# Kernel tuning notes

Measured on AMD Instinct MI355X. Metric: run time of the kernel, lower is better.

The kernel has to match this reference:

```python
import jax, jax.numpy as jnp
import numpy as np

B, L, D, MELS, VOCAB, MAXDUR = 16, 256, 512, 80, 256, 12
T_MAX = L * MAXDUR  # 3072, upper bound on expanded mel length


def setup_inputs() -> dict:
    key = jax.random.key(0)
    ks = jax.random.split(key, 10)
    s = 1.0 / np.sqrt(D)
    return {
        "src": jax.random.randint(ks[0], (B, L), 0, VOCAB),
        "input_dur_inframe": jax.random.randint(ks[1], (B, L), 0, MAXDUR),
        "T": T_MAX,
        "emb_table": jax.random.normal(ks[2], (VOCAB, D), jnp.float32),
        "pos_table": jax.random.normal(ks[3], (L, D), jnp.float32),
        "W_enc": jax.random.normal(ks[4], (D, D), jnp.float32) * s,
        "b_enc": jnp.zeros((D,), jnp.float32),
        "W_dur": jax.random.normal(ks[5], (D, 1), jnp.float32) * s,
        "b_dur": jnp.zeros((1,), jnp.float32),
        "W_dec": jax.random.normal(ks[6], (D, D), jnp.float32) * s,
        "b_dec": jnp.zeros((D,), jnp.float32),
        "W_gen": jax.random.normal(ks[7], (D, MELS), jnp.float32) * s,
        "b_gen": jnp.zeros((MELS,), jnp.float32),
    }


def length_regulate(enc, dur, T):
    """Vectorized equivalent of the nested per-(batch, token) scatter loop.
    Frame f of batch j copies enc[j, k] where k is the token whose duration
    span covers f; frames past the total duration stay zero."""
    csum = jnp.cumsum(dur, axis=-1)                      # [B, L]
    frames = jnp.arange(T)                               # [T]
    # token index per frame: count of tokens with csum <= f
    tok = jax.vmap(lambda c: jnp.searchsorted(c, frames, side="right"))(csum)  # [B, T]
    valid = (tok < dur.shape[1])[..., None]               # [B, T, 1]
    tok = jnp.minimum(tok, dur.shape[1] - 1)
    out = jnp.take_along_axis(enc, tok[..., None], axis=1)  # [B, T, D]
    return out * valid


def reference(src, input_dur_inframe, T, emb_table, pos_table,
              W_enc, b_enc, W_dur, b_dur, W_dec, b_dec, W_gen, b_gen):
    # encode: embedding + positional embedding -> encoder
    x = emb_table[src] + pos_table[None, : src.shape[1], :]        # [B, L, D]
    enc = jax.nn.relu(x @ W_enc + b_enc)                            # [B, L, D]
    # duration predictor on encoder output
    dur_pred = (enc @ W_dur + b_dur)[..., 0]                        # [B, L]
    # length regulator (the custom-kernel hot spot)
    outp = length_regulate(enc, input_dur_inframe, T)               # [B, T, D]
    # decoder + generator, then permute to [B, n_mels, T]
    dec = jax.nn.relu(outp @ W_dec + b_dec)                         # [B, T, D]
    mel = jnp.transpose(dec @ W_gen + b_gen, (0, 2, 1))             # [B, MELS, T]
    return mel, dur_pred
```

## Files before the change

kernel.cpp:

```cpp
#include <hip/hip_runtime.h>

#define D_ 512
#define L_ 256
#define B_ 16
#define T_ 3072
#define MELS_ 80
#define R_ 4096
#define CS_ 4104

typedef __bf16 bf16x8 __attribute__((ext_vector_type(8)));
typedef float f32x4 __attribute__((ext_vector_type(4)));

__device__ __forceinline__ unsigned f2bf(float f) {
  union { float f; unsigned u; } x; x.f = f;
  return (x.u + 0x7FFFu + ((x.u >> 16) & 1u)) >> 16;
}
__device__ __forceinline__ float bf2f(unsigned h) {
  union { unsigned u; float f; } x; x.u = h << 16;
  return x.f;
}

__device__ __forceinline__ void transw_dev(const float* __restrict__ src,
                                           unsigned short* __restrict__ dst,
                                           int N, int local, float* sh) {
  int kt = local & 7, nt = local >> 3;
  int k0 = kt * 64, n0 = nt * 64;
  int tid = threadIdx.x;
  int c = tid & 63, r4 = tid >> 6;
  for (int it = 0; it < 16; ++it) {
    int r = it * 4 + r4;
    int n = n0 + c;
    sh[r * 65 + c] = (n < N) ? src[(k0 + r) * N + n] : 0.f;
  }
  __syncthreads();
  for (int it = 0; it < 16; ++it) {
    int r = it * 4 + r4;
    int n = n0 + r;
    if (n < N) dst[n * D_ + k0 + c] = (unsigned short)f2bf(sh[c * 65 + r]);
  }
}

__device__ __forceinline__ void tok_dev(const int* __restrict__ dur,
                                        int* __restrict__ TOK, int b, int* cs) {
  int tid = threadIdx.x;
  cs[tid] = dur[b * L_ + tid];
  for (int off = 1; off < L_; off <<= 1) {
    __syncthreads();
    int v = (tid >= off) ? cs[tid - off] : 0;
    __syncthreads();
    cs[tid] += v;
  }
  __syncthreads();
  for (int t = tid; t < T_; t += 256) {
    int lo = 0, hi = L_;
    while (lo < hi) { int mid = (lo + hi) >> 1; if (cs[mid] <= t) lo = mid + 1; else hi = mid; }
    TOK[b * T_ + t] = (lo < L_) ? (b * L_ + lo) : R_;
  }
}

__device__ __forceinline__ void gemm_tile(
    const unsigned short* __restrict__ A, const unsigned short* __restrict__ Bt,
    const float* __restrict__ bias, unsigned short* __restrict__ C,
    int m0, int n0, int mclamp, int mstore, short* lsA, short* lsB) {
  int tid = threadIdx.x;
  int lane = tid & 63, w = tid >> 6;
  int wm = w >> 1, wn = w & 1;
  int col = lane & 15, quad = lane >> 4;
  f32x4 acc[2][2] = {};
  for (int ks = 0; ks < 4; ++ks) {
    int k0 = ks * 128;
    __syncthreads();
    for (int it = 0; it < 4; ++it) {
      int linear = it * 256 + tid;
      int row = linear >> 4, p = linear & 15;
      int seg = (p + row) & 15;
      const unsigned short* ga = A + (size_t)min(m0 + row, mclamp) * D_ + k0 + seg * 8;
      const unsigned short* gb = Bt + (size_t)(n0 + row) * D_ + k0 + seg * 8;
      short* la = lsA + (size_t)(it * 256 + (tid & ~63)) * 8;
      short* lb = lsB + (size_t)(it * 256 + (tid & ~63)) * 8;
      __builtin_amdgcn_global_load_lds((const __attribute__((address_space(1))) void*)ga,
                                       (__attribute__((address_space(3))) void*)la, 16, 0, 0);
      __builtin_amdgcn_global_load_lds((const __attribute__((address_space(1))) void*)gb,
                                       (__attribute__((address_space(3))) void*)lb, 16, 0, 0);
    }
    __syncthreads();
    for (int kk = 0; kk < 4; ++kk) {
      int s = kk * 4 + quad;
      bf16x8 af[2], bfr[2];
      for (int mt = 0; mt < 2; ++mt) {
        int r = wm * 32 + mt * 16 + col;
        af[mt] = *(const bf16x8*)(lsA + (size_t)r * 128 + ((s - r) & 15) * 8);
      }
      for (int nt = 0; nt < 2; ++nt) {
        int r = wn * 32 + nt * 16 + col;
        bfr[nt] = *(const bf16x8*)(lsB + (size_t)r * 128 + ((s - r) & 15) * 8);
      }
      for (int mt = 0; mt < 2; ++mt)
        for (int nt = 0; nt < 2; ++nt)
          acc[mt][nt] = __builtin_amdgcn_mfma_f32_16x16x32_bf16(af[mt], bfr[nt], acc[mt][nt], 0, 0, 0);
    }
  }
  for (int nt = 0; nt < 2; ++nt) {
    int n = n0 + wn * 32 + nt * 16 + col;
    float bn = bias[n];
    for (int mt = 0; mt < 2; ++mt) {
      int mb = m0 + wm * 32 + mt * 16 + quad * 4;
      for (int i = 0; i < 4; ++i) {
        int m = mb + i;
        if (m < mstore) {
          float v = acc[mt][nt][i] + bn;
          v = v > 0.f ? v : 0.f;
          C[(size_t)m * D_ + n] = (unsigned short)f2bf(v);
        }
      }
    }
  }
}

__global__ void prep1(const int* __restrict__ src, const float* __restrict__ emb,
                      const float* __restrict__ pos, const float* __restrict__ Wenc,
                      unsigned short* __restrict__ X, unsigned short* __restrict__ WET,
                      unsigned short* __restrict__ ENC) {
  __shared__ float sh[64 * 65];
  int bid = blockIdx.x, tid = threadIdx.x;
  if (bid < 512) {
    int lane = tid & 63, w = tid >> 6;
    for (int u = 0; u < 2; ++u) {
      int row = bid * 8 + u * 4 + w;
      int s = src[row];
      int l = row & (L_ - 1);
      int d = lane * 8;
      const float4* ep = (const float4*)(emb + (size_t)s * D_ + d);
      const float4* pp = (const float4*)(pos + (size_t)l * D_ + d);
      float4 a0 = ep[0], a1 = ep[1];
      float4 b0 = pp[0], b1 = pp[1];
      uint4 o;
      o.x = f2bf(a0.x + b0.x) | (f2bf(a0.y + b0.y) << 16);
      o.y = f2bf(a0.z + b0.z) | (f2bf(a0.w + b0.w) << 16);
      o.z = f2bf(a1.x + b1.x) | (f2bf(a1.y + b1.y) << 16);
      o.w = f2bf(a1.z + b1.z) | (f2bf(a1.w + b1.w) << 16);
      *(uint4*)(X + (size_t)row * D_ + d) = o;
    }
  } else if (bid < 576) {
    transw_dev(Wenc, WET, 512, bid - 512, sh);
  } else {
    if (tid < 64) {
      uint4 z = {0u, 0u, 0u, 0u};
      *(uint4*)(ENC + (size_t)R_ * D_ + (tid & 63) * 8) = z;
    }
  }
}

__global__ __launch_bounds__(256, 4) void gemm_enc(
    const unsigned short* __restrict__ X, const unsigned short* __restrict__ WET,
    const float* __restrict__ benc, unsigned short* __restrict__ ENC,
    const float* __restrict__ Wdec, const float* __restrict__ Wgen,
    const int* __restrict__ dur,
    unsigned short* __restrict__ WDT, unsigned short* __restrict__ WGT,
    int* __restrict__ TOK) {
  __shared__ __align__(16) char smem[32768];
  int bid = blockIdx.x;
  if (bid < 512) {
    gemm_tile(X, WET, benc, ENC, (bid >> 3) * 64, (bid & 7) * 64, R_ - 1, R_,
              (short*)smem, (short*)(smem + 16384));
  } else if (bid < 576) {
    transw_dev(Wdec, WDT, 512, bid - 512, (float*)smem);
  } else if (bid < 592) {
    transw_dev(Wgen, WGT, MELS_, bid - 576, (float*)smem);
  } else {
    tok_dev(dur, TOK, bid - 592, (int*)smem);
  }
}

__global__ __launch_bounds__(256, 4) void gemm_dec(
    const unsigned short* __restrict__ ENC, const unsigned short* __restrict__ WDT,
    const float* __restrict__ bdec, unsigned short* __restrict__ DEC,
    const float* __restrict__ wdur, const float* __restrict__ bdur,
    float* __restrict__ durout) {
  __shared__ __align__(16) char smem[32768];
  int bid = blockIdx.x, tid = threadIdx.x;
  int lane = tid & 63, w = tid >> 6;
  if (bid >= 520) {
    int b2 = bid - 520;
    float4 w0 = *(const float4*)(wdur + lane * 8);
    float4 w1 = *(const float4*)(wdur + lane * 8 + 4);
    float bv = bdur[0];
    for (int rep = 0; rep < 4; ++rep) {
      int row = b2 * 16 + w * 4 + rep;
      const uint4 e = *(const uint4*)(ENC + (size_t)row * D_ + lane * 8);
      float s = 0.f;
      s += bf2f(e.x & 0xffffu) * w0.x;  s += bf2f(e.x >> 16) * w0.y;
      s += bf2f(e.y & 0xffffu) * w0.z;  s += bf2f(e.y >> 16) * w0.w;
      s += bf2f(e.z & 0xffffu) * w1.x;  s += bf2f(e.z >> 16) * w1.y;
      s += bf2f(e.w & 0xffffu) * w1.z;  s += bf2f(e.w >> 16) * w1.w;
      for (int off = 32; off > 0; off >>= 1) s += __shfl_down(s, off, 64);
      if (lane == 0) durout[row] = s + bv;
    }
    return;
  }
  gemm_tile(ENC, WDT, bdec, DEC, (bid >> 3) * 64, (bid & 7) * 64, R_, R_ + 1,
            (short*)smem, (short*)(smem + 16384));
}

__global__ void genk(const unsigned short* __restrict__ dec, const unsigned short* __restrict__ wgT,
                     const float* __restrict__ bgen, float* __restrict__ melT) {
  __shared__ float sh[4 * 80 * 16];
  int tid = threadIdx.x;
  int lane = tid & 63, w = tid >> 6;
  int col = lane & 15, quad = lane >> 4;
  int n0 = blockIdx.x * 16;
  int n = n0 + col;
  int nc = min(n, R_);
  f32x4 acc[5] = {};
  const unsigned short* dp = dec + (size_t)nc * D_ + quad * 8;
  for (int ks = 0; ks < 4; ++ks) {
    int k0 = (w * 4 + ks) * 32;
    bf16x8 bfr = *(const bf16x8*)(dp + k0);
    for (int mt = 0; mt < 5; ++mt) {
      bf16x8 afr = *(const bf16x8*)(wgT + (size_t)(mt * 16 + col) * D_ + k0 + quad * 8);
      acc[mt] = __builtin_amdgcn_mfma_f32_16x16x32_bf16(afr, bfr, acc[mt], 0, 0, 0);
    }
  }
  for (int mt = 0; mt < 5; ++mt)
    for (int i = 0; i < 4; ++i)
      sh[w * 1280 + (mt * 16 + quad * 4 + i) * 16 + col] = acc[mt][i];
  __syncthreads();
  for (int j = 0; j < 5; ++j) {
    int idx = j * 256 + tid;
    float v = sh[idx] + sh[1280 + idx] + sh[2560 + idx] + sh[3840 + idx];
    int m = idx >> 4;
    int nn = n0 + (idx & 15);
    if (nn <= R_) melT[(size_t)m * CS_ + nn] = v + bgen[m];
  }
}

__global__ void outk(const int* __restrict__ TOK, const float* __restrict__ melT,
                     float* __restrict__ out) {
  int b = blockIdx.y;
  int tl = blockIdx.x * 128 + (threadIdx.x & 31) * 4;
  int m0 = threadIdx.x >> 5;
  int4 tg = *(const int4*)(TOK + b * T_ + tl);
  float* ob = out + (size_t)b * MELS_ * T_ + tl;
  for (int it = 0; it < 10; ++it) {
    int m = m0 + it * 8;
    const float* mr = melT + (size_t)m * CS_;
    float4 v = make_float4(mr[tg.x], mr[tg.y], mr[tg.z], mr[tg.w]);
    *(float4*)(ob + (size_t)m * T_) = v;
  }
}

extern "C" void kernel_launch(void* const* d_in, const int* in_sizes, int n_in,
                              void* d_out, int out_size, void* d_ws, size_t ws_size,
                              hipStream_t stream) {
  const int* src = (const int*)d_in[0];
  const int* dur = (const int*)d_in[1];
  const float* emb = (const float*)d_in[3];
  const float* pos = (const float*)d_in[4];
  const float* Wenc = (const float*)d_in[5];
  const float* benc = (const float*)d_in[6];
  const float* Wdur = (const float*)d_in[7];
  const float* bdur = (const float*)d_in[8];
  const float* Wdec = (const float*)d_in[9];
  const float* bdec = (const float*)d_in[10];
  const float* Wgen = (const float*)d_in[11];
  const float* bgen = (const float*)d_in[12];

  char* ws = (char*)d_ws;
  unsigned short* X   = (unsigned short*)(ws + 0);
  unsigned short* ENC = (unsigned short*)(ws + 4194304);
  unsigned short* DEC = (unsigned short*)(ws + 8389632);
  unsigned short* WET = (unsigned short*)(ws + 12584960);
  unsigned short* WDT = (unsigned short*)(ws + 13109248);
  unsigned short* WGT = (unsigned short*)(ws + 13633536);
  int* TOK            = (int*)(ws + 13715456);
  float* MELT         = (float*)(ws + 13912064);

  float* out = (float*)d_out;
  float* durout = out + (size_t)B_ * MELS_ * T_;

  prep1<<<577, 256, 0, stream>>>(src, emb, pos, Wenc, X, WET, ENC);
  gemm_enc<<<608, 256, 0, stream>>>(X, WET, benc, ENC, Wdec, Wgen, dur, WDT, WGT, TOK);
  gemm_dec<<<776, 256, 0, stream>>>(ENC, WDT, bdec, DEC, Wdur, bdur, durout);
  genk<<<257, 256, 0, stream>>>(DEC, WGT, bgen, MELT);
  outk<<<dim3(24, 16), 256, 0, stream>>>(TOK, MELT, out);
}
```

Baseline: 122.4 us.

## Double-buffer LDS tiles in gemm_tile to overlap global loads with MFMA

Splits tile staging into a helper and adds a second LDS buffer pair, so the next K-slice is prefetched with global_load_lds while MFMAs run on the current slice. The aim is to hide global-memory latency and drop one barrier per K step. Shared memory doubles to 64KB and the launch_bounds occupancy hint falls from 4 to 2, so fewer blocks fit per CU. The K loop only has 4 steps, which limits how much latency can be overlapped.

```diff
diff --git a/kernel.cpp b/kernel.cpp
--- a/kernel.cpp
+++ b/kernel.cpp
@@ -58,47 +58,68 @@
   }
 }
 
+__device__ __forceinline__ void stage_ab(
+    const unsigned short* __restrict__ A, const unsigned short* __restrict__ Bt,
+    int m0, int n0, int mclamp, int k0, short* lsA, short* lsB, int tid) {
+#pragma unroll
+  for (int it = 0; it < 4; ++it) {
+    int linear = it * 256 + tid;
+    int row = linear >> 4, p = linear & 15;
+    int seg = (p + row) & 15;
+    const unsigned short* ga = A + (size_t)min(m0 + row, mclamp) * D_ + k0 + seg * 8;
+    const unsigned short* gb = Bt + (size_t)(n0 + row) * D_ + k0 + seg * 8;
+    short* la = lsA + (size_t)(it * 256 + (tid & ~63)) * 8;
+    short* lb = lsB + (size_t)(it * 256 + (tid & ~63)) * 8;
+    __builtin_amdgcn_global_load_lds((const __attribute__((address_space(1))) void*)ga,
+                                     (__attribute__((address_space(3))) void*)la, 16, 0, 0);
+    __builtin_amdgcn_global_load_lds((const __attribute__((address_space(1))) void*)gb,
+                                     (__attribute__((address_space(3))) void*)lb, 16, 0, 0);
+  }
+}
+
 __device__ __forceinline__ void gemm_tile(
     const unsigned short* __restrict__ A, const unsigned short* __restrict__ Bt,
     const float* __restrict__ bias, unsigned short* __restrict__ C,
-    int m0, int n0, int mclamp, int mstore, short* lsA, short* lsB) {
+    int m0, int n0, int mclamp, int mstore, char* smem) {
+  short* lsA0 = (short*)smem;
+  short* lsB0 = (short*)(smem + 16384);
+  short* lsA1 = (short*)(smem + 32768);
+  short* lsB1 = (short*)(smem + 49152);
   int tid = threadIdx.x;
   int lane = tid & 63, w = tid >> 6;
   int wm = w >> 1, wn = w & 1;
   int col = lane & 15, quad = lane >> 4;
   f32x4 acc[2][2] = {};
+  stage_ab(A, Bt, m0, n0, mclamp, 0, lsA0, lsB0, tid);
+  __syncthreads();
+#pragma unroll
   for (int ks = 0; ks < 4; ++ks) {
-    int k0 = ks * 128;
-    __syncthreads();
-    for (int it = 0; it < 4; ++it) {
-      int linear = it * 256 + tid;
-      int row = linear >> 4, p = linear & 15;
-      int seg = (p + row) & 15;
-      const unsigned short* ga = A + (size_t)min(m0 + row, mclamp) * D_ + k0 + seg * 8;
-      const unsigned short* gb = Bt + (size_t)(n0 + row) * D_ + k0 + seg * 8;
-      short* la = lsA + (size_t)(it * 256 + (tid & ~63)) * 8;
-      short* lb = lsB + (size_t)(it * 256 + (tid & ~63)) * 8;
-      __builtin_amdgcn_global_load_lds((const __attribute__((address_space(1))) void*)ga,
-                                       (__attribute__((address_space(3))) void*)la, 16, 0, 0);
-      __builtin_amdgcn_global_load_lds((const __attribute__((address_space(1))) void*)gb,
-                                       (__attribute__((address_space(3))) void*)lb, 16, 0, 0);
-    }
-    __syncthreads();
+    short* cA = (ks & 1) ? lsA1 : lsA0;
+    short* cB = (ks & 1) ? lsB1 : lsB0;
+    short* nA = (ks & 1) ? lsA0 : lsA1;
+    short* nB = (ks & 1) ? lsB0 : lsB1;
+    if (ks < 3) stage_ab(A, Bt, m0, n0, mclamp, (ks + 1) * 128, nA, nB, tid);
+#pragma unroll
     for (int kk = 0; kk < 4; ++kk) {
       int s = kk * 4 + quad;
       bf16x8 af[2], bfr[2];
+#pragma unroll
       for (int mt = 0; mt < 2; ++mt) {
         int r = wm * 32 + mt * 16 + col;
-        af[mt] = *(const bf16x8*)(lsA + (size_t)r * 128 + ((s - r) & 15) * 8);
+        af[mt] = *(const bf16x8*)(cA + (size_t)r * 128 + ((s - r) & 15) * 8);
       }
+#pragma unroll
       for (int nt = 0; nt < 2; ++nt) {
         int r = wn * 32 + nt * 16 + col;
-        bfr[nt] = *(const bf16x8*)(lsB + (size_t)r * 128 + ((s - r) & 15) * 8);
+        bfr[nt] = *(const bf16x8*)(cB + (size_t)r * 128 + ((s - r) & 15) * 8);
       }
+#pragma unroll
       for (int mt = 0; mt < 2; ++mt)
+#pragma unroll
         for (int nt = 0; nt < 2; ++nt)
           acc[mt][nt] = __builtin_amdgcn_mfma_f32_16x16x32_bf16(af[mt], bfr[nt], acc[mt][nt], 0, 0, 0);
     }
+    if (ks < 3) __syncthreads();
   }
   for (int nt = 0; nt < 2; ++nt) {
     int n = n0 + wn * 32 + nt * 16 + col;
@@ -151,18 +172,17 @@
   }
 }
 
-__global__ __launch_bounds__(256, 4) void gemm_enc(
+__global__ __launch_bounds__(256, 2) void gemm_enc(
     const unsigned short* __restrict__ X, const unsigned short* __restrict__ WET,
     const float* __restrict__ benc, unsigned short* __restrict__ ENC,
     const float* __restrict__ Wdec, const float* __restrict__ Wgen,
     const int* __restrict__ dur,
     unsigned short* __restrict__ WDT, unsigned short* __restrict__ WGT,
     int* __restrict__ TOK) {
-  __shared__ __align__(16) char smem[32768];
+  __shared__ __align__(16) char smem[65536];
   int bid = blockIdx.x;
   if (bid < 512) {
-    gemm_tile(X, WET, benc, ENC, (bid >> 3) * 64, (bid & 7) * 64, R_ - 1, R_,
-              (short*)smem, (short*)(smem + 16384));
+    gemm_tile(X, WET, benc, ENC, (bid >> 3) * 64, (bid & 7) * 64, R_ - 1, R_, smem);
   } else if (bid < 576) {
     transw_dev(Wdec, WDT, 512, bid - 512, (float*)smem);
   } else if (bid < 592) {
@@ -172,12 +192,12 @@
   }
 }
 
-__global__ __launch_bounds__(256, 4) void gemm_dec(
+__global__ __launch_bounds__(256, 2) void gemm_dec(
     const unsigned short* __restrict__ ENC, const unsigned short* __restrict__ WDT,
     const float* __restrict__ bdec, unsigned short* __restrict__ DEC,
     const float* __restrict__ wdur, const float* __restrict__ bdur,
     float* __restrict__ durout) {
-  __shared__ __align__(16) char smem[32768];
+  __shared__ __align__(16) char smem[65536];
   int bid = blockIdx.x, tid = threadIdx.x;
   int lane = tid & 63, w = tid >> 6;
   if (bid >= 520) {
@@ -198,8 +218,7 @@
     }
     return;
   }
-  gemm_tile(ENC, WDT, bdec, DEC, (bid >> 3) * 64, (bid & 7) * 64, R_, R_ + 1,
-            (short*)smem, (short*)(smem + 16384));
+  gemm_tile(ENC, WDT, bdec, DEC, (bid >> 3) * 64, (bid & 7) * 64, R_, R_ + 1, smem);
 }
 
 __global__ void genk(const unsigned short* __restrict__ dec, const unsigned short* __restrict__ wgT,
```

Result: slower. 128.7 us (+5.1%).
